# Performance work log

Measured on AMD Instinct MI355X. Metric: run time of the kernel, lower is better.

## Reference

```python
import jax, jax.numpy as jnp
import numpy as np

INPUT, OUTPUT, HIDDEN, EMBED = 20000, 2048, 1024, 512
BATCH, NUM_GENES = 512, 20000

def _linear_init(key, fan_in, fan_out):
    kw, kb = jax.random.split(key)
    bound = 1.0 / np.sqrt(fan_in)
    W = jax.random.uniform(kw, (fan_out, fan_in), minval=-bound, maxval=bound, dtype=jnp.float32)
    b = jax.random.uniform(kb, (fan_out,), minval=-bound, maxval=bound, dtype=jnp.float32)
    return W, b

def setup_inputs() -> dict:
    key = jax.random.key(0)
    kx, ke, k1, k2, k3 = jax.random.split(key, 5)
    x = jax.random.normal(kx, (BATCH, INPUT), dtype=jnp.float32)
    embedding_x = jax.random.normal(ke, (NUM_GENES, EMBED), dtype=jnp.float32)
    W_ge, b_ge = _linear_init(k1, INPUT, HIDDEN)   # gene_expander Linear
    W_em, b_em = _linear_init(k2, EMBED, HIDDEN)   # embed_mlp Linear
    W_c, b_c = _linear_init(k3, 2 * HIDDEN, OUTPUT)  # combiner Linear
    return {"x": x, "embedding_x": embedding_x, "W_ge": W_ge, "b_ge": b_ge,
            "W_em": W_em, "b_em": b_em, "W_c": W_c, "b_c": b_c}

def reference(x, embedding_x, W_ge, b_ge, W_em, b_em, W_c, b_c):
    lrelu = lambda v: jax.nn.leaky_relu(v, negative_slope=0.01)
    # gene_expander: [B, input] -> [B, hidden]
    x_expanded = lrelu(x @ W_ge.T + b_ge)
    # embed_mlp (dropout = identity at eval): [G, embed] -> [G, hidden]
    gene_embeddings = lrelu(embedding_x @ W_em.T + b_em)
    # softmax over features, then batched GEMM replaces the per-sample loop
    num_genes = min(x.shape[1], gene_embeddings.shape[0])
    weights = jax.nn.softmax(x, axis=1)
    weighted_embeddings = weights[:, :num_genes] @ gene_embeddings[:num_genes]  # [B, hidden]
    combined = jnp.concatenate([x_expanded, weighted_embeddings], axis=1)  # [B, 2*hidden]
    return lrelu(combined @ W_c.T + b_c)  # [B, output]
```

## Files before the change

### kernel.cpp

```cpp
#include <hip/hip_runtime.h>
#include <hip/hip_bf16.h>
#include <stdint.h>

#define BATCH  512
#define INPUT  20000
#define KPAD   20032
#define NPADE  20224
#define HIDDEN 1024
#define EMBED  512
#define NOUT   2048

typedef __attribute__((ext_vector_type(8))) __bf16 bf16x8;
typedef __attribute__((ext_vector_type(8))) unsigned short u16x8;
typedef __attribute__((ext_vector_type(4))) unsigned short u16x4;
typedef __attribute__((ext_vector_type(4))) float f32x4;

static __device__ __forceinline__ unsigned short f2bf(float f) {
  uint32_t u = __builtin_bit_cast(uint32_t, f);
  u += 0x7fffu + ((u >> 16) & 1u);
  return (unsigned short)(u >> 16);
}

static __device__ __forceinline__ void g2l16(const unsigned short* g, unsigned short* l) {
  __builtin_amdgcn_global_load_lds(
      (const __attribute__((address_space(1))) void*)g,
      (__attribute__((address_space(3))) void*)l, 16, 0, 0);
}

#define MFMA(a, b, c) __builtin_amdgcn_mfma_f32_16x16x32_bf16((a), (b), (c), 0, 0, 0)

template<int EPI>
__global__ __launch_bounds__(256, 2) void gemmQ(
    const unsigned short* __restrict__ A0p, const unsigned short* __restrict__ B0p,
    const unsigned short* __restrict__ A1p, const unsigned short* __restrict__ B1p,
    int lda, int ldb,
    const float* __restrict__ bias,
    void* __restrict__ Cp, int ldc,
    int Nv, int Nw, int K, int kChunk)
{
  __shared__ __align__(16) unsigned short AsW[2 * 128 * 32];
  __shared__ __align__(16) unsigned short BsW[2 * 256 * 32];

  const int b = blockIdx.x;
  int m0, n0, z = 0, which = 0;
  if (EPI == 1) {
    int g = ((b >> 7) << 3) | (b & 7);
    int j = (b >> 3) & 15;
    which = g >> 4; z = g & 15;
    m0 = (j & 3) * 128;
    n0 = (j >> 2) * 256;
  } else {
    int xcd = b & 7, r = b >> 3;
    int m = r / 10, q = r - m * 10;
    int nidx = xcd + 8 * q;
    if (nidx >= 79) return;
    m0 = m * 128;
    n0 = nidx * 256;
  }
  const unsigned short* Ap = which ? A1p : A0p;
  const unsigned short* Bp = which ? B1p : B0p;

  const int k0   = z * kChunk;
  const int kend = min(K, k0 + kChunk);
  const int nt   = (kend - k0) >> 5;

  const int tid = threadIdx.x;
  const int l = tid & 63, w = tid >> 6;
  const int srow = tid >> 2;
  const int sc8  = tid & 3;
  const unsigned short* agl = Ap + (size_t)(m0 + srow) * lda + k0 + sc8 * 8;
  const unsigned short* bgl = Bp + (size_t)(n0 + srow) * ldb + k0 + sc8 * 8;
  const int swc = ((sc8 ^ ((srow >> 1) & 3)) << 3);

  const int lr = l & 15, lkc = l >> 4;
  const int ck = ((lkc ^ ((lr >> 1) & 3)) << 3);

  f32x4 acc[8][4] = {};
  u16x8 ra0, ra1, rb0, rb1, rb2, rb3;

#define LOADT(dk)                                                           \
  do {                                                                      \
    ra0 = *reinterpret_cast<const u16x8*>(agl + (size_t)0   * lda + (dk)); \
    ra1 = *reinterpret_cast<const u16x8*>(agl + (size_t)64  * lda + (dk)); \
    rb0 = *reinterpret_cast<const u16x8*>(bgl + (size_t)0   * ldb + (dk)); \
    rb1 = *reinterpret_cast<const u16x8*>(bgl + (size_t)64  * ldb + (dk)); \
    rb2 = *reinterpret_cast<const u16x8*>(bgl + (size_t)128 * ldb + (dk)); \
    rb3 = *reinterpret_cast<const u16x8*>(bgl + (size_t)192 * ldb + (dk)); \
  } while (0)

#define WRITET(BUF)                                                         \
  do {                                                                      \
    *reinterpret_cast<u16x8*>(AsW + (BUF)*4096 + (srow      ) * 32 + swc) = ra0; \
    *reinterpret_cast<u16x8*>(AsW + (BUF)*4096 + (srow +  64) * 32 + swc) = ra1; \
    *reinterpret_cast<u16x8*>(BsW + (BUF)*8192 + (srow      ) * 32 + swc) = rb0; \
    *reinterpret_cast<u16x8*>(BsW + (BUF)*8192 + (srow +  64) * 32 + swc) = rb1; \
    *reinterpret_cast<u16x8*>(BsW + (BUF)*8192 + (srow + 128) * 32 + swc) = rb2; \
    *reinterpret_cast<u16x8*>(BsW + (BUF)*8192 + (srow + 192) * 32 + swc) = rb3; \
  } while (0)

  LOADT(0);
  WRITET(0);
  __syncthreads();

  for (int t = 0; t < nt; ++t) {
    const int buf = t & 1, nb = buf ^ 1;
    if (t + 1 < nt) LOADT((t + 1) << 5);
    __builtin_amdgcn_sched_barrier(0);

    bf16x8 a[8], bfr[4];
#pragma unroll
    for (int mi = 0; mi < 8; ++mi)
      a[mi] = *reinterpret_cast<const bf16x8*>(AsW + buf * 4096 + (mi * 16 + lr) * 32 + ck);
#pragma unroll
    for (int ni = 0; ni < 4; ++ni)
      bfr[ni] = *reinterpret_cast<const bf16x8*>(
          BsW + buf * 8192 + (w * 64 + ni * 16 + lr) * 32 + ck);

    __builtin_amdgcn_s_setprio(1);
#pragma unroll
    for (int mi = 0; mi < 8; ++mi)
#pragma unroll
      for (int ni = 0; ni < 4; ++ni)
        acc[mi][ni] = MFMA(a[mi], bfr[ni], acc[mi][ni]);
    __builtin_amdgcn_s_setprio(0);

    if (t + 1 < nt) WRITET(nb);
    __syncthreads();
  }
#undef LOADT
#undef WRITET

  const int rb_ = (l >> 4) * 4;
#pragma unroll
  for (int mi = 0; mi < 8; ++mi)
#pragma unroll
    for (int ni = 0; ni < 4; ++ni)
#pragma unroll
      for (int j = 0; j < 4; ++j) {
        int m = m0 + mi * 16 + rb_ + j;
        int n = n0 + w * 64 + ni * 16 + lr;
        float v = acc[mi][ni][j];
        if (EPI == 0) {
          if (n < Nw) {
            float t2 = v + bias[m];
            t2 = t2 > 0.f ? t2 : 0.01f * t2;
            reinterpret_cast<unsigned short*>(Cp)[(size_t)m * ldc + n] =
                (n < Nv) ? f2bf(t2) : (unsigned short)0;
          }
        } else {
          reinterpret_cast<float*>(Cp)[(size_t)z * (BATCH * NOUT) + (size_t)m * ldc +
                                       which * 1024 + n] = v;
        }
      }
}

template<int EPI>
__global__ __launch_bounds__(256) void gemm97(
    const unsigned short* __restrict__ A, const unsigned short* __restrict__ B,
    int lda, int ldb,
    const float* __restrict__ bias,
    void* __restrict__ Cp, int ldc, int pstride,
    int M, int N, int Nw, int K, int kChunk)
{
  __shared__ __align__(16) unsigned short As[128 * 64];
  __shared__ __align__(16) unsigned short Bs[128 * 64];

  const int z = blockIdx.z;
  const int m0 = blockIdx.y * 128, n0 = blockIdx.x * 128;
  const int k0   = z * kChunk;
  const int kend = min(K, k0 + kChunk);
  const int tid = threadIdx.x;
  const int l = tid & 63, w = tid >> 6;

  const int srow = w * 32 + (l >> 3);
  const int scol = (l & 7) * 8;
  const unsigned short* ag = A + (size_t)(m0 + srow) * lda + scol;
  const unsigned short* bg = B + (size_t)(n0 + srow) * ldb + scol;

  const int wm = (w >> 1) * 64, wn = (w & 1) * 64;
  const int lr = l & 15, lk = (l >> 4) * 8;

  f32x4 acc[4][4] = {};

  for (int kb = k0; kb < kend; kb += 64) {
#pragma unroll
    for (int j = 0; j < 4; ++j)
      g2l16(ag + (size_t)j * 8 * lda + kb, As + (w * 32 + j * 8) * 64);
#pragma unroll
    for (int j = 0; j < 4; ++j)
      g2l16(bg + (size_t)j * 8 * ldb + kb, Bs + (w * 32 + j * 8) * 64);
    __syncthreads();
#pragma unroll
    for (int ks = 0; ks < 2; ++ks) {
      bf16x8 a[4], b2[4];
#pragma unroll
      for (int i = 0; i < 4; ++i)
        a[i] = *reinterpret_cast<const bf16x8*>(&As[(wm + i * 16 + lr) * 64 + ks * 32 + lk]);
#pragma unroll
      for (int i = 0; i < 4; ++i)
        b2[i] = *reinterpret_cast<const bf16x8*>(&Bs[(wn + i * 16 + lr) * 64 + ks * 32 + lk]);
#pragma unroll
      for (int mi = 0; mi < 4; ++mi)
#pragma unroll
        for (int ni = 0; ni < 4; ++ni)
          acc[mi][ni] = MFMA(a[mi], b2[ni], acc[mi][ni]);
    }
    __syncthreads();
  }

  const int rb = (l >> 4) * 4;
#pragma unroll
  for (int mi = 0; mi < 4; ++mi) {
#pragma unroll
    for (int ni = 0; ni < 4; ++ni) {
#pragma unroll
      for (int j = 0; j < 4; ++j) {
        int m = m0 + wm + mi * 16 + rb + j;
        int n = n0 + wn + ni * 16 + lr;
        float v = acc[mi][ni][j];
        if (EPI == 0) {
          if (n < Nw) {
            float t = v + bias[m];
            t = t > 0.f ? t : 0.01f * t;
            reinterpret_cast<unsigned short*>(Cp)[(size_t)m * ldc + n] =
                (n < N) ? f2bf(t) : (unsigned short)0;
          }
        } else {
          reinterpret_cast<float*>(Cp)[(size_t)z * pstride + (size_t)m * ldc + n] = v;
        }
      }
    }
  }
}

__global__ __launch_bounds__(256) void convert_kernel(
    const float* __restrict__ src, unsigned short* __restrict__ dst,
    int rows, int cols, int rowsPad, int colsPad)
{
  const int cpc = colsPad >> 3;
  const int nchunks = rowsPad * cpc;
  for (int idx = blockIdx.x * 256 + threadIdx.x; idx < nchunks; idx += gridDim.x * 256) {
    int row = idx / cpc;
    int c0  = (idx - row * cpc) << 3;
    u16x8 v = {};
    if (row < rows && c0 < cols) {
      const float* p = src + (size_t)row * cols + c0;
      f32x4 f0 = *reinterpret_cast<const f32x4*>(p);
      f32x4 f1 = *reinterpret_cast<const f32x4*>(p + 4);
      v[0] = f2bf(f0[0]); v[1] = f2bf(f0[1]); v[2] = f2bf(f0[2]); v[3] = f2bf(f0[3]);
      v[4] = f2bf(f1[0]); v[5] = f2bf(f1[1]); v[6] = f2bf(f1[2]); v[7] = f2bf(f1[3]);
    }
    *reinterpret_cast<u16x8*>(dst + (size_t)row * colsPad + c0) = v;
  }
}

__global__ __launch_bounds__(256) void prep_x_kernel(
    const float* __restrict__ x,
    unsigned short* __restrict__ xb,
    unsigned short* __restrict__ wb)
{
  const int r = blockIdx.x;
  const int t = threadIdx.x;
  const float* xr = x + (size_t)r * INPUT;

  float m = -3.4e38f, s = 0.f;
  for (int c = t; c < INPUT / 4; c += 256) {
    float4 v = reinterpret_cast<const float4*>(xr)[c];
    float cm = fmaxf(fmaxf(v.x, v.y), fmaxf(v.z, v.w));
    if (cm > m) { s *= __expf(m - cm); m = cm; }
    s += __expf(v.x - m) + __expf(v.y - m) + __expf(v.z - m) + __expf(v.w - m);
  }
#pragma unroll
  for (int off = 32; off > 0; off >>= 1) {
    float om = __shfl_xor(m, off);
    float os = __shfl_xor(s, off);
    float nm = fmaxf(m, om);
    s = s * __expf(m - nm) + os * __expf(om - nm);
    m = nm;
  }
  __shared__ float sm[4], ss[4];
  if ((t & 63) == 0) { sm[t >> 6] = m; ss[t >> 6] = s; }
  __syncthreads();
  float M4 = fmaxf(fmaxf(sm[0], sm[1]), fmaxf(sm[2], sm[3]));
  float S4 = ss[0] * __expf(sm[0] - M4) + ss[1] * __expf(sm[1] - M4)
           + ss[2] * __expf(sm[2] - M4) + ss[3] * __expf(sm[3] - M4);
  float inv = 1.f / S4;

  unsigned short* xbr = xb + (size_t)r * KPAD;
  unsigned short* wbr = wb + (size_t)r * KPAD;
  for (int c = t; c < KPAD / 4; c += 256) {
    u16x4 xo = {}, wo = {};
    if (c < INPUT / 4) {
      float4 v = reinterpret_cast<const float4*>(xr)[c];
      xo[0] = f2bf(v.x); xo[1] = f2bf(v.y); xo[2] = f2bf(v.z); xo[3] = f2bf(v.w);
      wo[0] = f2bf(__expf(v.x - M4) * inv);
      wo[1] = f2bf(__expf(v.y - M4) * inv);
      wo[2] = f2bf(__expf(v.z - M4) * inv);
      wo[3] = f2bf(__expf(v.w - M4) * inv);
    }
    reinterpret_cast<u16x4*>(xbr)[c] = xo;
    reinterpret_cast<u16x4*>(wbr)[c] = wo;
  }
}

template<int S, int MODE>
__global__ __launch_bounds__(256) void reduce_kernel(
    const float* __restrict__ P, const float* __restrict__ bias, void* __restrict__ outp)
{
  size_t base = ((size_t)blockIdx.x * 256 + threadIdx.x) * 4;
  f32x4 s = {};
#pragma unroll
  for (int zz = 0; zz < S; ++zz)
    s += *reinterpret_cast<const f32x4*>(P + (size_t)zz * BATCH * NOUT + base);
  int n = (int)(base & (NOUT - 1));
  if (MODE == 0) {
    u16x4 o;
    if (n < 1024) {
#pragma unroll
      for (int j = 0; j < 4; ++j) {
        float v = s[j] + bias[n + j];
        v = v > 0.f ? v : 0.01f * v;
        o[j] = f2bf(v);
      }
    } else {
#pragma unroll
      for (int j = 0; j < 4; ++j) o[j] = f2bf(s[j]);
    }
    *reinterpret_cast<u16x4*>(reinterpret_cast<unsigned short*>(outp) + base) = o;
  } else {
    f32x4 o;
#pragma unroll
    for (int j = 0; j < 4; ++j) {
      float v = s[j] + bias[n + j];
      o[j] = v > 0.f ? v : 0.01f * v;
    }
    *reinterpret_cast<f32x4*>(reinterpret_cast<float*>(outp) + base) = o;
  }
}

extern "C" void kernel_launch(void* const* d_in, const int* in_sizes, int n_in,
                              void* d_out, int out_size, void* d_ws, size_t ws_size,
                              hipStream_t stream)
{
  const float* x    = (const float*)d_in[0];
  const float* emb  = (const float*)d_in[1];
  const float* W_ge = (const float*)d_in[2];
  const float* b_ge = (const float*)d_in[3];
  const float* W_em = (const float*)d_in[4];
  const float* b_em = (const float*)d_in[5];
  const float* W_c  = (const float*)d_in[6];
  const float* b_c  = (const float*)d_in[7];
  float* out = (float*)d_out;

  char* ws = (char*)d_ws;
  unsigned short* xb   = (unsigned short*)(ws);
  unsigned short* wb   = (unsigned short*)(ws + 20512768);
  unsigned short* Wgeb = (unsigned short*)(ws + 41025536);
  unsigned short* Et   = (unsigned short*)(ws + 82051072);
  unsigned short* Wcb  = (unsigned short*)(ws + 123076608);
  unsigned short* comb = (unsigned short*)(ws + 131465216);
  float*          P    = (float*)(ws + 133562368);
  unsigned short* embb = (unsigned short*)(ws + 133562368);
  unsigned short* Wemb = (unsigned short*)(ws + 133562368 + 20709376);

  convert_kernel<<<1024, 256, 0, stream>>>(emb,  embb, INPUT, EMBED, NPADE, EMBED);
  convert_kernel<<<256,  256, 0, stream>>>(W_em, Wemb, HIDDEN, EMBED, HIDDEN, EMBED);
  convert_kernel<<<1024, 256, 0, stream>>>(W_ge, Wgeb, HIDDEN, INPUT, HIDDEN, KPAD);
  convert_kernel<<<512,  256, 0, stream>>>(W_c,  Wcb,  NOUT, NOUT, NOUT, NOUT);

  prep_x_kernel<<<BATCH, 256, 0, stream>>>(x, xb, wb);

  gemmQ<0><<<640, 256, 0, stream>>>(
      Wemb, embb, nullptr, nullptr, EMBED, EMBED, b_em,
      Et, KPAD, INPUT, KPAD, EMBED, EMBED);

  gemmQ<1><<<512, 256, 0, stream>>>(
      xb, Wgeb, wb, Et, KPAD, KPAD, nullptr,
      P, NOUT, 0, 0, KPAD, 1280);

  reduce_kernel<16, 0><<<(BATCH * NOUT / 4) / 256, 256, 0, stream>>>(P, b_ge, comb);

  gemm97<1><<<dim3(16, 4, 4), 256, 0, stream>>>(
      comb, Wcb, NOUT, NOUT, nullptr,
      P, NOUT, BATCH * NOUT, BATCH, NOUT, NOUT, NOUT, 512);

  reduce_kernel<4, 1><<<(BATCH * NOUT / 4) / 256, 256, 0, stream>>>(P, b_c, out);
}
```

Before: 229.7 us.

## Replace embed GEMM with A-resident LDS kernel streaming B from global

Adds a dedicated kernel for the embedding MLP GEMM that loads a full 64x512 slice of W_em into swizzled LDS once, then streams embedding rows directly from global memory into registers for MFMA, fusing bias and leaky ReLU into the transposed bf16 store. Blocks are mapped across XCDs so that each XCD shares the N range. This drops the generic double-buffered gemmQ<0> path and its K-loop LDS staging for B. The trade-off is heavier LDS use per block (64KB), which limits occupancy, plus uncoalesced-ish direct global B loads and a scalar transposed output store.

Measured after the change: 238.0 us. 1.04x slower.

```diff
diff --git a/kernel.cpp b/kernel.cpp
--- a/kernel.cpp
+++ b/kernel.cpp
@@ -28,6 +28,72 @@
 }
 
 #define MFMA(a, b, c) __builtin_amdgcn_mfma_f32_16x16x32_bf16((a), (b), (c), 0, 0, 0)
+
+__global__ __launch_bounds__(256, 2) void et_stream(
+    const unsigned short* __restrict__ Wemb, const unsigned short* __restrict__ embb,
+    const float* __restrict__ bias, unsigned short* __restrict__ Et)
+{
+  __shared__ __align__(16) unsigned short As[64 * 512];
+
+  const int b = blockIdx.x;
+  const int xcd = b & 7, rank = b >> 3;
+  const int mt = rank & 15;
+  const int q  = rank >> 4;
+  const int nidx = xcd + 8 * q;
+  if (nidx >= 79) return;
+  const int m0 = mt * 64, n0 = nidx * 256;
+
+  const int tid = threadIdx.x;
+  const int l = tid & 63, w = tid >> 6;
+  const int lr = l & 15, lkc = l >> 4;
+
+#pragma unroll
+  for (int i = 0; i < 16; ++i) {
+    int flat = i * 256 + tid;
+    int row = flat >> 6, ch = flat & 63;
+    u16x8 v = *reinterpret_cast<const u16x8*>(Wemb + (size_t)(m0 + row) * EMBED + ch * 8);
+    *reinterpret_cast<u16x8*>(As + row * EMBED + ((ch ^ (row & 7)) << 3)) = v;
+  }
+  __syncthreads();
+
+  const unsigned short* bbase = embb + (size_t)(n0 + w * 64 + lr) * EMBED + lkc * 8;
+
+  f32x4 acc[4][4] = {};
+#pragma unroll
+  for (int ks = 0; ks < 16; ++ks) {
+    bf16x8 bfr[4], a[4];
+#pragma unroll
+    for (int ni = 0; ni < 4; ++ni)
+      bfr[ni] = *reinterpret_cast<const bf16x8*>(bbase + (size_t)(ni * 16) * EMBED + ks * 32);
+#pragma unroll
+    for (int mi = 0; mi < 4; ++mi)
+      a[mi] = *reinterpret_cast<const bf16x8*>(
+          As + (mi * 16 + lr) * EMBED + (((ks * 4 + lkc) ^ (lr & 7)) << 3));
+    __builtin_amdgcn_s_setprio(1);
+#pragma unroll
+    for (int mi = 0; mi < 4; ++mi)
+#pragma unroll
+      for (int ni = 0; ni < 4; ++ni)
+        acc[mi][ni] = MFMA(a[mi], bfr[ni], acc[mi][ni]);
+    __builtin_amdgcn_s_setprio(0);
+  }
+
+  const int rb_ = (l >> 4) * 4;
+#pragma unroll
+  for (int mi = 0; mi < 4; ++mi)
+#pragma unroll
+    for (int ni = 0; ni < 4; ++ni)
+#pragma unroll
+      for (int j = 0; j < 4; ++j) {
+        int m = m0 + mi * 16 + rb_ + j;
+        int n = n0 + w * 64 + ni * 16 + lr;
+        if (n < KPAD) {
+          float t2 = acc[mi][ni][j] + bias[m];
+          t2 = t2 > 0.f ? t2 : 0.01f * t2;
+          Et[(size_t)m * KPAD + n] = (n < INPUT) ? f2bf(t2) : (unsigned short)0;
+        }
+      }
+}
 
 template<int EPI>
 __global__ __launch_bounds__(256, 2) void gemmQ(
@@ -370,9 +436,7 @@
 
   prep_x_kernel<<<BATCH, 256, 0, stream>>>(x, xb, wb);
 
-  gemmQ<0><<<640, 256, 0, stream>>>(
-      Wemb, embb, nullptr, nullptr, EMBED, EMBED, b_em,
-      Et, KPAD, INPUT, KPAD, EMBED, EMBED);
+  et_stream<<<1280, 256, 0, stream>>>(Wemb, embb, b_em, Et);
 
   gemmQ<1><<<512, 256, 0, stream>>>(
       xb, Wgeb, wb, Et, KPAD, KPAD, nullptr,
```

## Store GEMM operands in K-chunked tiled layout for contiguous tile loads

Applied to the files above, without the earlier changes.

Converts the bf16 operands (embedding, W_em, W_ge, x, softmax weights, and the intermediate Et) into a layout split into 32-wide K chunks, where each chunk stores all rows contiguously. The main GEMM kernel then loads each K-tile as one contiguous 64-byte-per-row block instead of strided rows across a 20032-element pitch. The goal is better DRAM/TLB locality and simpler address arithmetic in the large split-K GEMMs. Both the producer kernels and the GEMM indexing change to match, and the Et epilogue now writes with scattered tiled addressing.

Measured after the change: 233.2 us. Within noise of the previous version (+1.5%).

```diff
diff --git a/kernel.cpp b/kernel.cpp
--- a/kernel.cpp
+++ b/kernel.cpp
@@ -5,6 +5,7 @@
 #define BATCH  512
 #define INPUT  20000
 #define KPAD   20032
+#define KC_ALL 626
 #define NPADE  20224
 #define HIDDEN 1024
 #define EMBED  512
@@ -30,13 +31,13 @@
 #define MFMA(a, b, c) __builtin_amdgcn_mfma_f32_16x16x32_bf16((a), (b), (c), 0, 0, 0)
 
 template<int EPI>
-__global__ __launch_bounds__(256, 2) void gemmQ(
+__global__ __launch_bounds__(256, 2) void gemmP(
     const unsigned short* __restrict__ A0p, const unsigned short* __restrict__ B0p,
     const unsigned short* __restrict__ A1p, const unsigned short* __restrict__ B1p,
-    int lda, int ldb,
+    int RA, int RB,
     const float* __restrict__ bias,
-    void* __restrict__ Cp, int ldc,
-    int Nv, int Nw, int K, int kChunk)
+    void* __restrict__ Cp,
+    int Nv, int Nw, int KC, int CPZ)
 {
   __shared__ __align__(16) unsigned short AsW[2 * 128 * 32];
   __shared__ __align__(16) unsigned short BsW[2 * 256 * 32];
@@ -60,17 +61,18 @@
   const unsigned short* Ap = which ? A1p : A0p;
   const unsigned short* Bp = which ? B1p : B0p;
 
-  const int k0   = z * kChunk;
-  const int kend = min(K, k0 + kChunk);
-  const int nt   = (kend - k0) >> 5;
+  const int k0c = z * CPZ;
+  const int nt  = min(CPZ, KC - k0c);
 
   const int tid = threadIdx.x;
   const int l = tid & 63, w = tid >> 6;
   const int srow = tid >> 2;
   const int sc8  = tid & 3;
-  const unsigned short* agl = Ap + (size_t)(m0 + srow) * lda + k0 + sc8 * 8;
-  const unsigned short* bgl = Bp + (size_t)(n0 + srow) * ldb + k0 + sc8 * 8;
   const int swc = ((sc8 ^ ((srow >> 1) & 3)) << 3);
+
+  const size_t pa = (size_t)RA * 32, pb = (size_t)RB * 32;
+  const unsigned short* agl = Ap + (size_t)k0c * pa + (m0 + srow) * 32 + sc8 * 8;
+  const unsigned short* bgl = Bp + (size_t)k0c * pb + (n0 + srow) * 32 + sc8 * 8;
 
   const int lr = l & 15, lkc = l >> 4;
   const int ck = ((lkc ^ ((lr >> 1) & 3)) << 3);
@@ -78,18 +80,20 @@
   f32x4 acc[8][4] = {};
   u16x8 ra0, ra1, rb0, rb1, rb2, rb3;
 
-#define LOADT(dk)                                                           \
-  do {                                                                      \
-    ra0 = *reinterpret_cast<const u16x8*>(agl + (size_t)0   * lda + (dk)); \
-    ra1 = *reinterpret_cast<const u16x8*>(agl + (size_t)64  * lda + (dk)); \
-    rb0 = *reinterpret_cast<const u16x8*>(bgl + (size_t)0   * ldb + (dk)); \
-    rb1 = *reinterpret_cast<const u16x8*>(bgl + (size_t)64  * ldb + (dk)); \
-    rb2 = *reinterpret_cast<const u16x8*>(bgl + (size_t)128 * ldb + (dk)); \
-    rb3 = *reinterpret_cast<const u16x8*>(bgl + (size_t)192 * ldb + (dk)); \
+#define LOADT(ct)                                                               \
+  do {                                                                          \
+    const unsigned short* ab = agl + (size_t)(ct) * pa;                         \
+    const unsigned short* bb = bgl + (size_t)(ct) * pb;                         \
+    ra0 = *reinterpret_cast<const u16x8*>(ab);                                  \
+    ra1 = *reinterpret_cast<const u16x8*>(ab + 64 * 32);                        \
+    rb0 = *reinterpret_cast<const u16x8*>(bb);                                  \
+    rb1 = *reinterpret_cast<const u16x8*>(bb + 64 * 32);                        \
+    rb2 = *reinterpret_cast<const u16x8*>(bb + 128 * 32);                       \
+    rb3 = *reinterpret_cast<const u16x8*>(bb + 192 * 32);                       \
   } while (0)
 
-#define WRITET(BUF)                                                         \
-  do {                                                                      \
+#define WRITET(BUF)                                                             \
+  do {                                                                          \
     *reinterpret_cast<u16x8*>(AsW + (BUF)*4096 + (srow      ) * 32 + swc) = ra0; \
     *reinterpret_cast<u16x8*>(AsW + (BUF)*4096 + (srow +  64) * 32 + swc) = ra1; \
     *reinterpret_cast<u16x8*>(BsW + (BUF)*8192 + (srow      ) * 32 + swc) = rb0; \
@@ -104,7 +108,7 @@
 
   for (int t = 0; t < nt; ++t) {
     const int buf = t & 1, nb = buf ^ 1;
-    if (t + 1 < nt) LOADT((t + 1) << 5);
+    if (t + 1 < nt) LOADT(t + 1);
     __builtin_amdgcn_sched_barrier(0);
 
     bf16x8 a[8], bfr[4];
@@ -144,11 +148,12 @@
           if (n < Nw) {
             float t2 = v + bias[m];
             t2 = t2 > 0.f ? t2 : 0.01f * t2;
-            reinterpret_cast<unsigned short*>(Cp)[(size_t)m * ldc + n] =
+            reinterpret_cast<unsigned short*>(Cp)[
+                ((size_t)(n >> 5) * HIDDEN + m) * 32 + (n & 31)] =
                 (n < Nv) ? f2bf(t2) : (unsigned short)0;
           }
         } else {
-          reinterpret_cast<float*>(Cp)[(size_t)z * (BATCH * NOUT) + (size_t)m * ldc +
+          reinterpret_cast<float*>(Cp)[(size_t)z * (BATCH * NOUT) + (size_t)m * NOUT +
                                        which * 1024 + n] = v;
         }
       }
@@ -233,6 +238,28 @@
   }
 }
 
+__global__ __launch_bounds__(256) void convert_tiled_kernel(
+    const float* __restrict__ src, unsigned short* __restrict__ dst,
+    int rows, int cols, int rowsPad, int colsPad)
+{
+  const int cpc = colsPad >> 3;
+  const int nchunks = rowsPad * cpc;
+  for (int idx = blockIdx.x * 256 + threadIdx.x; idx < nchunks; idx += gridDim.x * 256) {
+    int row = idx / cpc;
+    int c8  = idx - row * cpc;
+    int c0  = c8 << 3;
+    u16x8 v = {};
+    if (row < rows && c0 < cols) {
+      const float* p = src + (size_t)row * cols + c0;
+      f32x4 f0 = *reinterpret_cast<const f32x4*>(p);
+      f32x4 f1 = *reinterpret_cast<const f32x4*>(p + 4);
+      v[0] = f2bf(f0[0]); v[1] = f2bf(f0[1]); v[2] = f2bf(f0[2]); v[3] = f2bf(f0[3]);
+      v[4] = f2bf(f1[0]); v[5] = f2bf(f1[1]); v[6] = f2bf(f1[2]); v[7] = f2bf(f1[3]);
+    }
+    *reinterpret_cast<u16x8*>(dst + ((size_t)(c0 >> 5) * rowsPad + row) * 32 + (c0 & 31)) = v;
+  }
+}
+
 __global__ __launch_bounds__(256) void convert_kernel(
     const float* __restrict__ src, unsigned short* __restrict__ dst,
     int rows, int cols, int rowsPad, int colsPad)
@@ -286,20 +313,24 @@
            + ss[2] * __expf(sm[2] - M4) + ss[3] * __expf(sm[3] - M4);
   float inv = 1.f / S4;
 
-  unsigned short* xbr = xb + (size_t)r * KPAD;
-  unsigned short* wbr = wb + (size_t)r * KPAD;
-  for (int c = t; c < KPAD / 4; c += 256) {
-    u16x4 xo = {}, wo = {};
-    if (c < INPUT / 4) {
-      float4 v = reinterpret_cast<const float4*>(xr)[c];
-      xo[0] = f2bf(v.x); xo[1] = f2bf(v.y); xo[2] = f2bf(v.z); xo[3] = f2bf(v.w);
-      wo[0] = f2bf(__expf(v.x - M4) * inv);
-      wo[1] = f2bf(__expf(v.y - M4) * inv);
-      wo[2] = f2bf(__expf(v.z - M4) * inv);
-      wo[3] = f2bf(__expf(v.w - M4) * inv);
-    }
-    reinterpret_cast<u16x4*>(xbr)[c] = xo;
-    reinterpret_cast<u16x4*>(wbr)[c] = wo;
+  for (int c8 = t; c8 < KPAD / 8; c8 += 256) {
+    int c0 = c8 << 3;
+    u16x8 xo = {}, wo = {};
+    if (c0 < INPUT) {
+      const float* p = xr + c0;
+      f32x4 f0 = *reinterpret_cast<const f32x4*>(p);
+      f32x4 f1 = *reinterpret_cast<const f32x4*>(p + 4);
+#pragma unroll
+      for (int j = 0; j < 4; ++j) {
+        xo[j]     = f2bf(f0[j]);
+        xo[j + 4] = f2bf(f1[j]);
+        wo[j]     = f2bf(__expf(f0[j] - M4) * inv);
+        wo[j + 4] = f2bf(__expf(f1[j] - M4) * inv);
+      }
+    }
+    size_t off = ((size_t)(c0 >> 5) * BATCH + r) * 32 + (c0 & 31);
+    *reinterpret_cast<u16x8*>(xb + off) = xo;
+    *reinterpret_cast<u16x8*>(wb + off) = wo;
   }
 }
 
@@ -353,30 +384,30 @@
   float* out = (float*)d_out;
 
   char* ws = (char*)d_ws;
-  unsigned short* xb   = (unsigned short*)(ws);
-  unsigned short* wb   = (unsigned short*)(ws + 20512768);
-  unsigned short* Wgeb = (unsigned short*)(ws + 41025536);
-  unsigned short* Et   = (unsigned short*)(ws + 82051072);
-  unsigned short* Wcb  = (unsigned short*)(ws + 123076608);
-  unsigned short* comb = (unsigned short*)(ws + 131465216);
-  float*          P    = (float*)(ws + 133562368);
-  unsigned short* embb = (unsigned short*)(ws + 133562368);
-  unsigned short* Wemb = (unsigned short*)(ws + 133562368 + 20709376);
-
-  convert_kernel<<<1024, 256, 0, stream>>>(emb,  embb, INPUT, EMBED, NPADE, EMBED);
-  convert_kernel<<<256,  256, 0, stream>>>(W_em, Wemb, HIDDEN, EMBED, HIDDEN, EMBED);
-  convert_kernel<<<1024, 256, 0, stream>>>(W_ge, Wgeb, HIDDEN, INPUT, HIDDEN, KPAD);
-  convert_kernel<<<512,  256, 0, stream>>>(W_c,  Wcb,  NOUT, NOUT, NOUT, NOUT);
-
-  prep_x_kernel<<<BATCH, 256, 0, stream>>>(x, xb, wb);
-
-  gemmQ<0><<<640, 256, 0, stream>>>(
-      Wemb, embb, nullptr, nullptr, EMBED, EMBED, b_em,
-      Et, KPAD, INPUT, KPAD, EMBED, EMBED);
-
-  gemmQ<1><<<512, 256, 0, stream>>>(
-      xb, Wgeb, wb, Et, KPAD, KPAD, nullptr,
-      P, NOUT, 0, 0, KPAD, 1280);
+  unsigned short* xb_t   = (unsigned short*)(ws);
+  unsigned short* wb_t   = (unsigned short*)(ws + 20512768);
+  unsigned short* Wgeb_t = (unsigned short*)(ws + 41025536);
+  unsigned short* Et_t   = (unsigned short*)(ws + 82051072);
+  unsigned short* Wcb    = (unsigned short*)(ws + 123076608);
+  unsigned short* comb   = (unsigned short*)(ws + 131465216);
+  float*          P      = (float*)(ws + 133562368);
+  unsigned short* embb_t = (unsigned short*)(ws + 133562368);
+  unsigned short* Wemb_t = (unsigned short*)(ws + 133562368 + 20709376);
+
+  convert_tiled_kernel<<<1024, 256, 0, stream>>>(emb,  embb_t, INPUT, EMBED, NPADE, EMBED);
+  convert_tiled_kernel<<<256,  256, 0, stream>>>(W_em, Wemb_t, HIDDEN, EMBED, HIDDEN, EMBED);
+  convert_tiled_kernel<<<1024, 256, 0, stream>>>(W_ge, Wgeb_t, HIDDEN, INPUT, HIDDEN, KPAD);
+  convert_kernel<<<512,  256, 0, stream>>>(W_c, Wcb, NOUT, NOUT, NOUT, NOUT);
+
+  prep_x_kernel<<<BATCH, 256, 0, stream>>>(x, xb_t, wb_t);
+
+  gemmP<0><<<640, 256, 0, stream>>>(
+      Wemb_t, embb_t, nullptr, nullptr, HIDDEN, NPADE, b_em,
+      Et_t, INPUT, KPAD, 16, 16);
+
+  gemmP<1><<<512, 256, 0, stream>>>(
+      xb_t, Wgeb_t, wb_t, Et_t, BATCH, HIDDEN, nullptr,
+      P, 0, 0, KC_ALL, 40);
 
   reduce_kernel<16, 0><<<(BATCH * NOUT / 4) / 256, 256, 0, stream>>>(P, b_ge, comb);
 
```
